# Kernel tuning notes

Measured on AMD Instinct MI355X. Metric: run time of the kernel, lower is better.

The kernel has to match this reference:

```python
import jax, jax.numpy as jnp
import numpy as np

B, IN, N, E = 2048, 1024, 64, 128
NEG_SLOPE = 0.01  # torch LeakyReLU default

def setup_inputs() -> dict:
    key = jax.random.key(0)
    k = jax.random.split(key, 5)
    scale_in = 1.0 / np.sqrt(IN)
    scale_ctx = 1.0 / np.sqrt(2 * E)
    return {
        "x": jax.random.normal(k[0], (B, IN), dtype=jnp.float32),
        # stacked per-concept Linear(in_features, 2*emb_size)
        "W_ctx": jax.random.uniform(k[1], (N, IN, 2 * E), jnp.float32, -scale_in, scale_in),
        "b_ctx": jax.random.uniform(k[2], (N, 2 * E), jnp.float32, -scale_in, scale_in),
        # shared Linear(2*emb_size, 1)
        "w_prob": jax.random.uniform(k[3], (2 * E,), jnp.float32, -scale_ctx, scale_ctx),
        "b_prob": jax.random.uniform(k[4], (), jnp.float32, -scale_ctx, scale_ctx),
    }

def reference(x, W_ctx, b_ctx, w_prob, b_prob):
    # context: [B, N, 2E] = LeakyReLU(x @ W_i + b_i) for all concepts i at once
    ctx = jnp.einsum("bi,nio->bno", x, W_ctx) + b_ctx
    ctx = jnp.where(ctx >= 0, ctx, NEG_SLOPE * ctx)
    # shared gate: [B, N]
    c_pred = jax.nn.sigmoid(jnp.einsum("bno,o->bn", ctx, w_prob) + b_prob)
    # gated blend of positive/negative halves -> [B, N, E]
    p = c_pred[..., None]
    c_emb = ctx[..., :E] * p + ctx[..., E:] * (1.0 - p)
    return c_emb, c_pred
```

## Files before the change

kernel.cpp:

```cpp
#include <hip/hip_runtime.h>
#include <hip/hip_bf16.h>

typedef __attribute__((ext_vector_type(8))) short short8v;
typedef __attribute__((ext_vector_type(4))) float floatx4;

#define B_ROWS 2048
#define K_DIM  1024
#define N_CON  64
#define TWO_E  256
#define E_DIM  128
#define BM     128
#define BK     64
#define LDSA_BYTES (BM * BK * 2)
#define LDSB_BYTES (TWO_E * BK * 2)
#define SMEM_BYTES (LDSA_BYTES + LDSB_BYTES)
#define EMB_ELEMS 16777216ULL
#define WT_BYTES  33554432ULL
#define XB_BYTES  4194304ULL

static __device__ inline unsigned short bf16bits(float f) {
    __hip_bfloat16 h = __float2bfloat16(f);
    unsigned short u;
    __builtin_memcpy(&u, &h, 2);
    return u;
}

static __device__ inline void dma16(const void* g, void* l) {
    __builtin_amdgcn_global_load_lds(
        (const __attribute__((address_space(1))) unsigned int*)g,
        (__attribute__((address_space(3))) unsigned int*)l,
        16, 0, 0);
}

__global__ void __launch_bounds__(256) prep(const float* __restrict__ W,
                                            const float* __restrict__ x,
                                            unsigned short* __restrict__ Wt,
                                            unsigned short* __restrict__ xb) {
    __shared__ unsigned int lds2[64 * 36];
    const int tid = threadIdx.x;
    const int ot = blockIdx.x, ktile = blockIdx.y, n = blockIdx.z;
    const float* src = W + ((size_t)n * K_DIM + (size_t)ktile * 64) * TWO_E + ot * 64;
    unsigned short* dst = Wt + ((size_t)n * TWO_E + (size_t)ot * 64) * K_DIM + ktile * 64;

    const int kp = tid >> 4;
    const int c  = (tid & 15) * 4;
#pragma unroll
    for (int it = 0; it < 2; ++it) {
        const int k0 = it * 32 + kp * 2;
        floatx4 r0 = *(const floatx4*)&src[(size_t)k0 * TWO_E + c];
        floatx4 r1 = *(const floatx4*)&src[(size_t)(k0 + 1) * TWO_E + c];
#pragma unroll
        for (int j = 0; j < 4; ++j) {
            unsigned int d = (unsigned int)bf16bits(r0[j]) |
                             ((unsigned int)bf16bits(r1[j]) << 16);
            lds2[(c + j) * 36 + it * 16 + kp] = d;
        }
    }
    __syncthreads();
#pragma unroll
    for (int it = 0; it < 2; ++it) {
        int q = it * 256 + tid;
        int o = q >> 3, kc = q & 7;
        short8v v = *(short8v*)&lds2[o * 36 + kc * 4];
        *(short8v*)&dst[(size_t)o * K_DIM + kc * 8] = v;
    }

    const int bid = blockIdx.x + blockIdx.y * 4 + blockIdx.z * 64;
    const size_t base = (size_t)bid * 512 + (size_t)tid * 2;
    unsigned int d = (unsigned int)bf16bits(x[base]) |
                     ((unsigned int)bf16bits(x[base + 1]) << 16);
    ((unsigned int*)xb)[base >> 1] = d;
}

__global__ void __launch_bounds__(256, 2)
concept4(const unsigned short* __restrict__ xb,
         const unsigned short* __restrict__ Wt,
         const float* __restrict__ bc,
         const float* __restrict__ wp,
         const float* __restrict__ bp,
         float* __restrict__ out) {
    __shared__ __align__(16) char smem[SMEM_BYTES];
    char* ldsA = smem;
    char* ldsB = smem + LDSA_BYTES;

    const int tid  = threadIdx.x;
    const int wave = tid >> 6;
    const int lane = tid & 63;
    const int lg   = lane >> 4;
    const int l15  = lane & 15;
    const int og   = wave;

    const int lin = blockIdx.y * 16 + blockIdx.x;
    const int nid = (lin & 7) * 128 + (lin >> 3);
    const int rb  = nid & 15;
    const int n   = nid >> 4;

    int otile[4];
#pragma unroll
    for (int oi = 0; oi < 4; ++oi) otile[oi] = og * 32 + (oi & 1) * 16 + (oi & 2) * 64;

    floatx4 acc[8][4];
#pragma unroll
    for (int mi = 0; mi < 8; ++mi)
#pragma unroll
        for (int oi = 0; oi < 4; ++oi) acc[mi][oi] = (floatx4){0.f, 0.f, 0.f, 0.f};

    const unsigned short* xrow  = xb + (size_t)rb * BM * K_DIM;
    const unsigned short* wbase = Wt + (size_t)n * TWO_E * K_DIM;

    for (int kt = 0; kt < K_DIM; kt += BK) {
#pragma unroll
        for (int it = 0; it < 4; ++it) {
            int c = it * 4 + wave;
            int s = c * 64 + lane;
            int r = s >> 3, g = s & 7;
            dma16(xrow + (size_t)r * K_DIM + kt + ((g ^ (r & 7)) * 8),
                  ldsA + c * 1024);
        }
#pragma unroll
        for (int it = 0; it < 8; ++it) {
            int c = it * 4 + wave;
            int s = c * 64 + lane;
            int r = s >> 3, g = s & 7;
            dma16(wbase + (size_t)r * K_DIM + kt + ((g ^ (r & 7)) * 8),
                  ldsB + c * 1024);
        }
        __syncthreads();

        short8v afA[4][2], afB[4][2], bf[2][2], bf2[2][2];

#pragma unroll
        for (int ks = 0; ks < 2; ++ks) {
            const int sw = ((ks * 4 + lg) ^ (l15 & 7)) * 16;
#pragma unroll
            for (int mi = 0; mi < 4; ++mi)
                afA[mi][ks] = *(const short8v*)(ldsA + (mi * 16 + l15) * 128 + sw);
#pragma unroll
            for (int oi = 0; oi < 2; ++oi)
                bf[oi][ks] = *(const short8v*)(ldsB + (otile[oi] + l15) * 128 + sw);
        }
#pragma unroll
        for (int mi = 0; mi < 4; ++mi)
#pragma unroll
            for (int oi = 0; oi < 2; ++oi)
#pragma unroll
                for (int ks = 0; ks < 2; ++ks)
                    acc[mi][oi] = __builtin_amdgcn_mfma_f32_16x16x32_bf16(
                        afA[mi][ks], bf[oi][ks], acc[mi][oi], 0, 0, 0);

#pragma unroll
        for (int ks = 0; ks < 2; ++ks) {
            const int sw = ((ks * 4 + lg) ^ (l15 & 7)) * 16;
#pragma unroll
            for (int oi = 0; oi < 2; ++oi)
                bf2[oi][ks] = *(const short8v*)(ldsB + (otile[2 + oi] + l15) * 128 + sw);
        }
#pragma unroll
        for (int mi = 0; mi < 4; ++mi)
#pragma unroll
            for (int oi = 0; oi < 2; ++oi)
#pragma unroll
                for (int ks = 0; ks < 2; ++ks)
                    acc[mi][2 + oi] = __builtin_amdgcn_mfma_f32_16x16x32_bf16(
                        afA[mi][ks], bf2[oi][ks], acc[mi][2 + oi], 0, 0, 0);

#pragma unroll
        for (int ks = 0; ks < 2; ++ks) {
            const int sw = ((ks * 4 + lg) ^ (l15 & 7)) * 16;
#pragma unroll
            for (int mi = 0; mi < 4; ++mi)
                afB[mi][ks] = *(const short8v*)(ldsA + (64 + mi * 16 + l15) * 128 + sw);
        }
#pragma unroll
        for (int mi = 0; mi < 4; ++mi)
#pragma unroll
            for (int oi = 0; oi < 2; ++oi)
#pragma unroll
                for (int ks = 0; ks < 2; ++ks)
                    acc[4 + mi][2 + oi] = __builtin_amdgcn_mfma_f32_16x16x32_bf16(
                        afB[mi][ks], bf2[oi][ks], acc[4 + mi][2 + oi], 0, 0, 0);

#pragma unroll
        for (int mi = 0; mi < 4; ++mi)
#pragma unroll
            for (int oi = 0; oi < 2; ++oi)
#pragma unroll
                for (int ks = 0; ks < 2; ++ks)
                    acc[4 + mi][oi] = __builtin_amdgcn_mfma_f32_16x16x32_bf16(
                        afB[mi][ks], bf[oi][ks], acc[4 + mi][oi], 0, 0, 0);

        __syncthreads();
    }

    float biasf[4], wpf[4];
#pragma unroll
    for (int oi = 0; oi < 4; ++oi) {
        int o = otile[oi] + l15;
        biasf[oi] = bc[n * TWO_E + o];
        wpf[oi]  = wp[o];
    }
#pragma unroll
    for (int mi = 0; mi < 8; ++mi)
#pragma unroll
        for (int oi = 0; oi < 4; ++oi)
#pragma unroll
            for (int j = 0; j < 4; ++j) {
                float v = acc[mi][oi][j] + biasf[oi];
                acc[mi][oi][j] = v >= 0.f ? v : 0.01f * v;
            }

    float* partial = (float*)smem;
    float* pv      = (float*)(smem + 2048);

#pragma unroll
    for (int mi = 0; mi < 8; ++mi)
#pragma unroll
        for (int j = 0; j < 4; ++j) {
            float ps = 0.f;
#pragma unroll
            for (int oi = 0; oi < 4; ++oi) ps += acc[mi][oi][j] * wpf[oi];
            ps += __shfl_xor(ps, 1);
            ps += __shfl_xor(ps, 2);
            ps += __shfl_xor(ps, 4);
            ps += __shfl_xor(ps, 8);
            if (l15 == 0) partial[(mi * 16 + lg * 4 + j) * 4 + og] = ps;
        }
    __syncthreads();

    if (tid < 128) {
        float s = partial[tid * 4] + partial[tid * 4 + 1] + partial[tid * 4 + 2] +
                  partial[tid * 4 + 3] + bp[0];
        float p = 1.f / (1.f + __expf(-s));
        pv[tid] = p;
        size_t bi = (size_t)rb * BM + tid;
        out[EMB_ELEMS + bi * N_CON + n] = p;
    }
    __syncthreads();

#pragma unroll
    for (int mi = 0; mi < 8; ++mi)
#pragma unroll
        for (int oi = 0; oi < 2; ++oi)
#pragma unroll
            for (int j = 0; j < 4; ++j) {
                int row = mi * 16 + lg * 4 + j;
                int e = og * 32 + oi * 16 + l15;
                float p = pv[row];
                float v = acc[mi][oi][j] * p + acc[mi][oi + 2][j] * (1.f - p);
                size_t bi = (size_t)rb * BM + row;
                out[(bi * N_CON + n) * E_DIM + e] = v;
            }
}

__global__ void __launch_bounds__(512, 4)
concept_fallback(const float* __restrict__ x,
                 const float* __restrict__ Wc,
                 const float* __restrict__ bc,
                 const float* __restrict__ wp,
                 const float* __restrict__ bp,
                 float* __restrict__ out) {
    __shared__ __align__(16) char smem[SMEM_BYTES];
    char* ldsA = smem;
    char* ldsB = smem + LDSA_BYTES;

    const int tid  = threadIdx.x;
    const int wave = tid >> 6;
    const int lane = tid & 63;
    const int lg   = lane >> 4;
    const int l15  = lane & 15;
    const int h    = wave >> 2;
    const int og   = wave & 3;
    const int rb = blockIdx.x;
    const int n  = blockIdx.y;

    int otile[4];
#pragma unroll
    for (int oi = 0; oi < 4; ++oi) otile[oi] = og * 32 + (oi & 1) * 16 + (oi & 2) * 64;

    floatx4 acc[4][4];
#pragma unroll
    for (int mi = 0; mi < 4; ++mi)
#pragma unroll
        for (int oi = 0; oi < 4; ++oi) acc[mi][oi] = (floatx4){0.f, 0.f, 0.f, 0.f};

    const float* xg = x + (size_t)rb * BM * K_DIM;
    const float* wg = Wc + (size_t)n * K_DIM * TWO_E;

    for (int kt = 0; kt < K_DIM; kt += BK) {
#pragma unroll
        for (int it = 0; it < 2; ++it) {
            int s = it * 512 + tid;
            int r = s >> 3, g = s & 7;
            const float* p = xg + (size_t)r * K_DIM + kt + ((g ^ (r & 7)) * 8);
            floatx4 v0 = *(const floatx4*)p, v1 = *(const floatx4*)(p + 4);
            short8v b;
            b[0] = (short)bf16bits(v0[0]); b[1] = (short)bf16bits(v0[1]);
            b[2] = (short)bf16bits(v0[2]); b[3] = (short)bf16bits(v0[3]);
            b[4] = (short)bf16bits(v1[0]); b[5] = (short)bf16bits(v1[1]);
            b[6] = (short)bf16bits(v1[2]); b[7] = (short)bf16bits(v1[3]);
            *(short8v*)(ldsA + s * 16) = b;
        }
#pragma unroll
        for (int it = 0; it < 4; ++it) {
            int s = it * 512 + tid;
            int r = s >> 3, g = s & 7;
            int k0 = kt + (g ^ (r & 7)) * 8;
            short8v b;
#pragma unroll
            for (int j = 0; j < 8; ++j)
                b[j] = (short)bf16bits(wg[(size_t)(k0 + j) * TWO_E + r]);
            *(short8v*)(ldsB + s * 16) = b;
        }
        __syncthreads();

#pragma unroll
        for (int ks = 0; ks < 2; ++ks) {
            const int sw = ((ks * 4 + lg) ^ (l15 & 7)) * 16;
            short8v af[4], bfr[4];
#pragma unroll
            for (int mi = 0; mi < 4; ++mi)
                af[mi] = *(const short8v*)(ldsA + (h * 64 + mi * 16 + l15) * 128 + sw);
#pragma unroll
            for (int oi = 0; oi < 4; ++oi)
                bfr[oi] = *(const short8v*)(ldsB + (otile[oi] + l15) * 128 + sw);
#pragma unroll
            for (int mi = 0; mi < 4; ++mi)
#pragma unroll
                for (int oi = 0; oi < 4; ++oi)
                    acc[mi][oi] = __builtin_amdgcn_mfma_f32_16x16x32_bf16(
                        af[mi], bfr[oi], acc[mi][oi], 0, 0, 0);
        }
        __syncthreads();
    }

    float biasf[4], wpf[4];
#pragma unroll
    for (int oi = 0; oi < 4; ++oi) {
        int o = otile[oi] + l15;
        biasf[oi] = bc[n * TWO_E + o];
        wpf[oi]  = wp[o];
    }
#pragma unroll
    for (int mi = 0; mi < 4; ++mi)
#pragma unroll
        for (int oi = 0; oi < 4; ++oi)
#pragma unroll
            for (int j = 0; j < 4; ++j) {
                float v = acc[mi][oi][j] + biasf[oi];
                acc[mi][oi][j] = v >= 0.f ? v : 0.01f * v;
            }

    float* partial = (float*)smem;
    float* pv      = (float*)(smem + 2048);

#pragma unroll
    for (int mi = 0; mi < 4; ++mi)
#pragma unroll
        for (int j = 0; j < 4; ++j) {
            float ps = 0.f;
#pragma unroll
            for (int oi = 0; oi < 4; ++oi) ps += acc[mi][oi][j] * wpf[oi];
            ps += __shfl_xor(ps, 1);
            ps += __shfl_xor(ps, 2);
            ps += __shfl_xor(ps, 4);
            ps += __shfl_xor(ps, 8);
            if (l15 == 0) partial[(h * 64 + mi * 16 + lg * 4 + j) * 4 + og] = ps;
        }
    __syncthreads();

    if (tid < 128) {
        float s = partial[tid * 4] + partial[tid * 4 + 1] + partial[tid * 4 + 2] +
                  partial[tid * 4 + 3] + bp[0];
        float p = 1.f / (1.f + __expf(-s));
        pv[tid] = p;
        size_t bi = (size_t)rb * BM + tid;
        out[EMB_ELEMS + bi * N_CON + n] = p;
    }
    __syncthreads();

#pragma unroll
    for (int mi = 0; mi < 4; ++mi)
#pragma unroll
        for (int oi = 0; oi < 2; ++oi)
#pragma unroll
            for (int j = 0; j < 4; ++j) {
                int row = h * 64 + mi * 16 + lg * 4 + j;
                int e = og * 32 + oi * 16 + l15;
                float p = pv[row];
                float v = acc[mi][oi][j] * p + acc[mi][oi + 2][j] * (1.f - p);
                size_t bi = (size_t)rb * BM + row;
                out[(bi * N_CON + n) * E_DIM + e] = v;
            }
}

extern "C" void kernel_launch(void* const* d_in, const int* in_sizes, int n_in,
                              void* d_out, int out_size, void* d_ws, size_t ws_size,
                              hipStream_t stream) {
    const float* x  = (const float*)d_in[0];
    const float* Wc = (const float*)d_in[1];
    const float* bc = (const float*)d_in[2];
    const float* wp = (const float*)d_in[3];
    const float* bp = (const float*)d_in[4];
    float* out = (float*)d_out;

    if (ws_size >= WT_BYTES + XB_BYTES) {
        unsigned short* Wt = (unsigned short*)d_ws;
        unsigned short* xb = (unsigned short*)((char*)d_ws + WT_BYTES);
        prep<<<dim3(4, 16, 64), 256, 0, stream>>>(Wc, x, Wt, xb);
        concept4<<<dim3(16, 64), 256, 0, stream>>>(xb, Wt, bc, wp, bp, out);
    } else {
        concept_fallback<<<dim3(16, 64), 512, 0, stream>>>(
            x, Wc, bc, wp, bp, out);
    }
}
```

Measured before the change: 192.6 us.

## Load W fragments directly into registers and double-buffer x tiles in LDS

Each wave now reads its own W operand fragments straight from global memory into registers instead of staging the whole W tile through LDS. Only the x tile stays in LDS, now double-buffered so the next tile's async load overlaps the current MFMA work, with one barrier per iteration. LDS use drops from 48KB to 32KB. In exchange, W reads become per-lane 16-byte global loads whose latency sits directly in front of the MFMAs, with no prefetch across iterations.

```diff
diff --git a/kernel.cpp b/kernel.cpp
--- a/kernel.cpp
+++ b/kernel.cpp
@@ -11,9 +11,9 @@
 #define E_DIM  128
 #define BM     128
 #define BK     64
+#define NT     16
 #define LDSA_BYTES (BM * BK * 2)
-#define LDSB_BYTES (TWO_E * BK * 2)
-#define SMEM_BYTES (LDSA_BYTES + LDSB_BYTES)
+#define SMEM_BYTES (2 * LDSA_BYTES)
 #define EMB_ELEMS 16777216ULL
 #define WT_BYTES  33554432ULL
 #define XB_BYTES  4194304ULL
@@ -73,15 +73,13 @@
 }
 
 __global__ void __launch_bounds__(256, 2)
-concept4(const unsigned short* __restrict__ xb,
+concept5(const unsigned short* __restrict__ xb,
          const unsigned short* __restrict__ Wt,
          const float* __restrict__ bc,
          const float* __restrict__ wp,
          const float* __restrict__ bp,
          float* __restrict__ out) {
     __shared__ __align__(16) char smem[SMEM_BYTES];
-    char* ldsA = smem;
-    char* ldsB = smem + LDSA_BYTES;
 
     const int tid  = threadIdx.x;
     const int wave = tid >> 6;
@@ -105,89 +103,62 @@
 #pragma unroll
         for (int oi = 0; oi < 4; ++oi) acc[mi][oi] = (floatx4){0.f, 0.f, 0.f, 0.f};
 
-    const unsigned short* xrow  = xb + (size_t)rb * BM * K_DIM;
-    const unsigned short* wbase = Wt + (size_t)n * TWO_E * K_DIM;
-
-    for (int kt = 0; kt < K_DIM; kt += BK) {
-#pragma unroll
-        for (int it = 0; it < 4; ++it) {
-            int c = it * 4 + wave;
-            int s = c * 64 + lane;
-            int r = s >> 3, g = s & 7;
-            dma16(xrow + (size_t)r * K_DIM + kt + ((g ^ (r & 7)) * 8),
-                  ldsA + c * 1024);
-        }
-#pragma unroll
-        for (int it = 0; it < 8; ++it) {
-            int c = it * 4 + wave;
-            int s = c * 64 + lane;
-            int r = s >> 3, g = s & 7;
-            dma16(wbase + (size_t)r * K_DIM + kt + ((g ^ (r & 7)) * 8),
-                  ldsB + c * 1024);
-        }
-        __syncthreads();
-
-        short8v afA[4][2], afB[4][2], bf[2][2], bf2[2][2];
-
-#pragma unroll
-        for (int ks = 0; ks < 2; ++ks) {
-            const int sw = ((ks * 4 + lg) ^ (l15 & 7)) * 16;
-#pragma unroll
-            for (int mi = 0; mi < 4; ++mi)
-                afA[mi][ks] = *(const short8v*)(ldsA + (mi * 16 + l15) * 128 + sw);
-#pragma unroll
-            for (int oi = 0; oi < 2; ++oi)
-                bf[oi][ks] = *(const short8v*)(ldsB + (otile[oi] + l15) * 128 + sw);
-        }
-#pragma unroll
-        for (int mi = 0; mi < 4; ++mi)
-#pragma unroll
-            for (int oi = 0; oi < 2; ++oi)
-#pragma unroll
-                for (int ks = 0; ks < 2; ++ks)
-                    acc[mi][oi] = __builtin_amdgcn_mfma_f32_16x16x32_bf16(
-                        afA[mi][ks], bf[oi][ks], acc[mi][oi], 0, 0, 0);
-
-#pragma unroll
-        for (int ks = 0; ks < 2; ++ks) {
-            const int sw = ((ks * 4 + lg) ^ (l15 & 7)) * 16;
-#pragma unroll
-            for (int oi = 0; oi < 2; ++oi)
-                bf2[oi][ks] = *(const short8v*)(ldsB + (otile[2 + oi] + l15) * 128 + sw);
-        }
-#pragma unroll
-        for (int mi = 0; mi < 4; ++mi)
-#pragma unroll
-            for (int oi = 0; oi < 2; ++oi)
-#pragma unroll
-                for (int ks = 0; ks < 2; ++ks)
-                    acc[mi][2 + oi] = __builtin_amdgcn_mfma_f32_16x16x32_bf16(
-                        afA[mi][ks], bf2[oi][ks], acc[mi][2 + oi], 0, 0, 0);
-
-#pragma unroll
-        for (int ks = 0; ks < 2; ++ks) {
-            const int sw = ((ks * 4 + lg) ^ (l15 & 7)) * 16;
-#pragma unroll
-            for (int mi = 0; mi < 4; ++mi)
-                afB[mi][ks] = *(const short8v*)(ldsA + (64 + mi * 16 + l15) * 128 + sw);
-        }
-#pragma unroll
-        for (int mi = 0; mi < 4; ++mi)
-#pragma unroll
-            for (int oi = 0; oi < 2; ++oi)
-#pragma unroll
-                for (int ks = 0; ks < 2; ++ks)
-                    acc[4 + mi][2 + oi] = __builtin_amdgcn_mfma_f32_16x16x32_bf16(
-                        afB[mi][ks], bf2[oi][ks], acc[4 + mi][2 + oi], 0, 0, 0);
-
-#pragma unroll
-        for (int mi = 0; mi < 4; ++mi)
-#pragma unroll
-            for (int oi = 0; oi < 2; ++oi)
-#pragma unroll
-                for (int ks = 0; ks < 2; ++ks)
-                    acc[4 + mi][oi] = __builtin_amdgcn_mfma_f32_16x16x32_bf16(
-                        afB[mi][ks], bf[oi][ks], acc[4 + mi][oi], 0, 0, 0);
+    const unsigned short* xrow = xb + (size_t)rb * BM * K_DIM;
+    const unsigned short* wb[4];
+#pragma unroll
+    for (int oi = 0; oi < 4; ++oi)
+        wb[oi] = Wt + ((size_t)n * TWO_E + otile[oi] + l15) * K_DIM + lg * 8;
+
+    const int sw0 = ((lg) ^ (l15 & 7)) * 16;
+    const int sw1 = ((4 + lg) ^ (l15 & 7)) * 16;
+    const int abase = l15 * 128;
+
+#pragma unroll
+    for (int it = 0; it < 4; ++it) {
+        int c = it * 4 + wave;
+        int s = c * 64 + lane;
+        int r = s >> 3, g = s & 7;
+        dma16(xrow + (size_t)r * K_DIM + ((g ^ (r & 7)) * 8), smem + c * 1024);
+    }
+    __syncthreads();
+
+#pragma unroll 1
+    for (int t = 0; t < NT; ++t) {
+        const int kt = t * BK;
+        char* ldsR = smem + (t & 1) * LDSA_BYTES;
+
+        short8v bfr[4][2];
+#pragma unroll
+        for (int oi = 0; oi < 4; ++oi)
+#pragma unroll
+            for (int ks = 0; ks < 2; ++ks)
+                bfr[oi][ks] = *(const short8v*)(wb[oi] + kt + ks * 32);
+
+        if (t + 1 < NT) {
+            char* ldsW = smem + ((t + 1) & 1) * LDSA_BYTES;
+            const int ktn = kt + BK;
+#pragma unroll
+            for (int it = 0; it < 4; ++it) {
+                int c = it * 4 + wave;
+                int s = c * 64 + lane;
+                int r = s >> 3, g = s & 7;
+                dma16(xrow + (size_t)r * K_DIM + ktn + ((g ^ (r & 7)) * 8),
+                      ldsW + c * 1024);
+            }
+        }
+
+#pragma unroll
+        for (int mi = 0; mi < 8; ++mi) {
+            short8v a0 = *(const short8v*)(ldsR + abase + mi * 2048 + sw0);
+            short8v a1 = *(const short8v*)(ldsR + abase + mi * 2048 + sw1);
+#pragma unroll
+            for (int oi = 0; oi < 4; ++oi) {
+                acc[mi][oi] = __builtin_amdgcn_mfma_f32_16x16x32_bf16(
+                    a0, bfr[oi][0], acc[mi][oi], 0, 0, 0);
+                acc[mi][oi] = __builtin_amdgcn_mfma_f32_16x16x32_bf16(
+                    a1, bfr[oi][1], acc[mi][oi], 0, 0, 0);
+            }
+        }
 
         __syncthreads();
     }
@@ -259,9 +230,9 @@
                  const float* __restrict__ wp,
                  const float* __restrict__ bp,
                  float* __restrict__ out) {
-    __shared__ __align__(16) char smem[SMEM_BYTES];
+    __shared__ __align__(16) char smem[49152];
     char* ldsA = smem;
-    char* ldsB = smem + LDSA_BYTES;
+    char* ldsB = smem + 16384;
 
     const int tid  = threadIdx.x;
     const int wave = tid >> 6;
@@ -407,7 +378,7 @@
         unsigned short* Wt = (unsigned short*)d_ws;
         unsigned short* xb = (unsigned short*)((char*)d_ws + WT_BYTES);
         prep<<<dim3(4, 16, 64), 256, 0, stream>>>(Wc, x, Wt, xb);
-        concept4<<<dim3(16, 64), 256, 0, stream>>>(xb, Wt, bc, wp, bp, out);
+        concept5<<<dim3(16, 64), 256, 0, stream>>>(xb, Wt, bc, wp, bp, out);
     } else {
         concept_fallback<<<dim3(16, 64), 512, 0, stream>>>(
             x, Wc, bc, wp, bp, out);
```

Measured after the change: 212.4 us. +10.2%, slower.
